# Optimization experiments

Hardware: AMD Instinct MI355X
Metric: run time of the kernel (lower is better)

The kernel has to match this reference:

```python
import jax, jax.numpy as jnp
import numpy as np

B, L, E, DA, R = 256, 2048, 64, 64, 32

def setup_inputs() -> dict:
    key = jax.random.key(0)
    k1, k2, k3, k4 = jax.random.split(key, 4)
    x = jax.random.normal(k1, (B, L, E), dtype=jnp.float32)
    mask = (jax.random.uniform(k2, (B, L)) > 0.2).astype(jnp.float32)
    # glorot-uniform-like init for the small attention weights
    lim1 = np.sqrt(6.0 / (DA + E)).astype(np.float32)
    lim2 = np.sqrt(6.0 / (R + DA)).astype(np.float32)
    W1 = jax.random.uniform(k3, (DA, E), minval=-lim1, maxval=lim1, dtype=jnp.float32)
    W2 = jax.random.uniform(k4, (R, DA), minval=-lim2, maxval=lim2, dtype=jnp.float32)
    return {"x": x, "mask": mask, "W1": W1, "W2": W2}

def reference(x, mask, W1, W2):
    # x: (B,L,E), mask: (B,L), W1: (DA,E), W2: (R,DA)
    xm = x * mask[:, :, None]                       # masked inputs (B,L,E)
    H = jnp.tanh(jnp.einsum('de,ble->bdl', W1, xm))  # (B,DA,L)
    Q = jnp.einsum('rd,bdl->brl', W2, H)             # (B,R,L)
    A = jnp.exp(Q) * mask[:, None, :]                # masked exp scores (B,R,L)
    A = A / jnp.sum(A, axis=2, keepdims=True)        # normalize over L
    # dropout is identity at inference
    return jnp.einsum('brl,ble->bre', A, xm)         # (B,R,E)
```

## Files before the change

kernel.cpp:

```cpp
#include <hip/hip_runtime.h>
#include <hip/hip_bf16.h>


#define B_  256
#define L_  2048
#define E_  64
#define DA_ 64
#define R_  32
#define CH_ 8
#define TL_ 128
#define NS_ 2

typedef __attribute__((ext_vector_type(8))) short bf16x8;
typedef __attribute__((ext_vector_type(4))) float f32x4;

#define XS_WROW 36
#define XT_WROW 68
#define AS_WROW 68
#define XS_WORDS (TL_ * XS_WROW)
#define XT_WORDS (E_ * XT_WROW)
#define AS_WORDS (R_ * AS_WROW)

__device__ __forceinline__ unsigned pk(float a, float b) {
    __hip_bfloat162 h = __float22bfloat162_rn(float2{a, b});
    union { __hip_bfloat162 h2; unsigned u; } cv; cv.h2 = h;
    return cv.u;
}
__device__ __forceinline__ float bflo(unsigned u) { return __uint_as_float(u << 16); }
__device__ __forceinline__ float bfhi(unsigned u) { return __uint_as_float(u & 0xFFFF0000u); }
__device__ __forceinline__ float fast_tanh(float v) {
    float e = __expf(2.0f * v);
    return 1.0f - 2.0f / (e + 1.0f);
}

__launch_bounds__(256, 3)
__global__ void selfbi_main(const float* __restrict__ x,
                            const float* __restrict__ mask,
                            const float* __restrict__ W1,
                            const float* __restrict__ W2,
                            float* __restrict__ accp,
                            float* __restrict__ ssump) {
    __shared__ unsigned smem[XS_WORDS + XT_WORDS + AS_WORDS + TL_];
    unsigned* xsw = smem;
    unsigned* xtw = smem + XS_WORDS;
    unsigned* asw = xtw + XT_WORDS;
    float*    ms  = (float*)(asw + AS_WORDS);

    const int b   = blockIdx.x;
    const int c   = blockIdx.y;
    const int tid = threadIdx.x;
    const int w    = tid >> 6;
    const int lane = tid & 63;
    const int g    = lane >> 4;
    const int ml   = lane & 15;

    bf16x8 w1f[4][2], w2f[2][2];
    #pragma unroll
    for (int mt = 0; mt < 4; ++mt)
        #pragma unroll
        for (int kb = 0; kb < 2; ++kb) {
            const float* p = W1 + (16 * mt + ml) * E_ + 32 * kb + 8 * g;
            float4 a = *(const float4*)p, bb = *(const float4*)(p + 4);
            union { bf16x8 s; unsigned u[4]; } cv;
            cv.u[0] = pk(a.x, a.y); cv.u[1] = pk(a.z, a.w);
            cv.u[2] = pk(bb.x, bb.y); cv.u[3] = pk(bb.z, bb.w);
            w1f[mt][kb] = cv.s;
        }
    #pragma unroll
    for (int mt = 0; mt < 2; ++mt)
        #pragma unroll
        for (int kb = 0; kb < 2; ++kb) {
            const float* p = W2 + (16 * mt + ml) * DA_ + 32 * kb + 8 * g;
            float4 a = *(const float4*)p, bb = *(const float4*)(p + 4);
            union { bf16x8 s; unsigned u[4]; } cv;
            cv.u[0] = pk(a.x, a.y); cv.u[1] = pk(a.z, a.w);
            cv.u[2] = pk(bb.x, bb.y); cv.u[3] = pk(bb.z, bb.w);
            w2f[mt][kb] = cv.s;
        }

    f32x4 c3[2] = {f32x4{0,0,0,0}, f32x4{0,0,0,0}};
    float ssum_acc = 0.0f;

    for (int s = 0; s < NS_; ++s) {
        if (s) __syncthreads();

        {
            const int t = tid >> 1, half = tid & 1;
            const int gl = b * L_ + c * (NS_ * TL_) + s * TL_ + t;
            const float m = mask[gl];
            if (!half) ms[t] = m;
            const float4* xr = (const float4*)(x + (size_t)gl * E_ + half * 32);
            float v[32];
            #pragma unroll
            for (int i = 0; i < 8; ++i) {
                float4 q = xr[i];
                v[4*i] = q.x * m; v[4*i+1] = q.y * m; v[4*i+2] = q.z * m; v[4*i+3] = q.w * m;
            }
            #pragma unroll
            for (int i = 0; i < 4; ++i) {
                uint4 u;
                u.x = pk(v[8*i+0], v[8*i+1]); u.y = pk(v[8*i+2], v[8*i+3]);
                u.z = pk(v[8*i+4], v[8*i+5]); u.w = pk(v[8*i+6], v[8*i+7]);
                *(uint4*)&xsw[t * XS_WROW + half * 16 + 4 * i] = u;
            }
            #pragma unroll
            for (int j = 0; j < 32; ++j) {
                const int e = 32 * half + j;
                const int word = e * XT_WROW + ((t >> 1) ^ (half << 4));
                ((__hip_bfloat16*)&xtw[word])[t & 1] = __float2bfloat16(v[j]);
            }
        }

        f32x4 c1[2][4];
        #pragma unroll
        for (int nt = 0; nt < 2; ++nt)
            #pragma unroll
            for (int mt = 0; mt < 4; ++mt) c1[nt][mt] = f32x4{0,0,0,0};
        #pragma unroll
        for (int kb = 0; kb < 2; ++kb)
            #pragma unroll
            for (int nt = 0; nt < 2; ++nt) {
                const int t = 32 * w + 16 * nt + ml;
                bf16x8 bfrag = *(bf16x8*)&xsw[t * XS_WROW + kb * 16 + 4 * g];
                #pragma unroll
                for (int mt = 0; mt < 4; ++mt)
                    c1[nt][mt] = __builtin_amdgcn_mfma_f32_16x16x32_bf16(
                        w1f[mt][kb], bfrag, c1[nt][mt], 0, 0, 0);
            }

        #pragma unroll
        for (int nt = 0; nt < 2; ++nt) {
            const int t = 32 * w + 16 * nt + ml;
            const int sw = 4 * (t & 7);
            #pragma unroll
            for (int mt = 0; mt < 4; ++mt) {
                float h0 = fast_tanh(c1[nt][mt][0]);
                float h1 = fast_tanh(c1[nt][mt][1]);
                float h2 = fast_tanh(c1[nt][mt][2]);
                float h3 = fast_tanh(c1[nt][mt][3]);
                const int d2 = 8 * mt + 2 * g;
                uint2 u; u.x = pk(h0, h1); u.y = pk(h2, h3);
                *(uint2*)&xsw[t * XS_WROW + (d2 ^ sw)] = u;
            }
        }

        f32x4 c2[2][2];
        #pragma unroll
        for (int nt = 0; nt < 2; ++nt)
            #pragma unroll
            for (int mt = 0; mt < 2; ++mt) c2[nt][mt] = f32x4{0,0,0,0};
        #pragma unroll
        for (int kb = 0; kb < 2; ++kb)
            #pragma unroll
            for (int nt = 0; nt < 2; ++nt) {
                const int t = 32 * w + 16 * nt + ml;
                const int sw = 4 * (t & 7);
                bf16x8 bfrag = *(bf16x8*)&xsw[t * XS_WROW + ((16 * kb + 4 * g) ^ sw)];
                #pragma unroll
                for (int mt = 0; mt < 2; ++mt)
                    c2[nt][mt] = __builtin_amdgcn_mfma_f32_16x16x32_bf16(
                        w2f[mt][kb], bfrag, c2[nt][mt], 0, 0, 0);
            }

        #pragma unroll
        for (int nt = 0; nt < 2; ++nt) {
            const int t = 32 * w + 16 * nt + ml;
            const float mval = ms[t];
            const int tw = (t >> 1) ^ (8 * g);
            #pragma unroll
            for (int mt = 0; mt < 2; ++mt)
                #pragma unroll
                for (int reg = 0; reg < 4; ++reg) {
                    const int r = 16 * mt + 4 * g + reg;
                    float a = __expf(c2[nt][mt][reg]) * mval;
                    ((__hip_bfloat16*)&asw[r * AS_WROW + tw])[t & 1] = __float2bfloat16(a);
                }
        }

        __syncthreads();

        {
            const int fx = (w >> 1) << 4;
            const int e  = 16 * w + ml;
            const int phi = 8 * ((ml >> 2) & 3);
            #pragma unroll
            for (int kb = 0; kb < 4; ++kb) {
                bf16x8 bfrag = *(bf16x8*)&xtw[e * XT_WROW + ((16 * kb + 4 * g) ^ fx)];
                #pragma unroll
                for (int mt = 0; mt < 2; ++mt) {
                    const int r = 16 * mt + ml;
                    bf16x8 afrag = *(bf16x8*)&asw[r * AS_WROW + ((16 * kb + 4 * g) ^ phi)];
                    c3[mt] = __builtin_amdgcn_mfma_f32_16x16x32_bf16(
                        afrag, bfrag, c3[mt], 0, 0, 0);
                }
            }
        }

        {
            const int rr = tid >> 3, to = tid & 7;
            const int p2 = (rr >> 2) & 3;
            const int wb = rr * AS_WROW + 8 * (to ^ p2);
            uint4 u0 = *(uint4*)&asw[wb];
            uint4 u1 = *(uint4*)&asw[wb + 4];
            float sv = bflo(u0.x) + bfhi(u0.x) + bflo(u0.y) + bfhi(u0.y)
                     + bflo(u0.z) + bfhi(u0.z) + bflo(u0.w) + bfhi(u0.w)
                     + bflo(u1.x) + bfhi(u1.x) + bflo(u1.y) + bfhi(u1.y)
                     + bflo(u1.z) + bfhi(u1.z) + bflo(u1.w) + bfhi(u1.w);
            ssum_acc += sv;
        }
    }

    float sv = ssum_acc;
    sv += __shfl_xor(sv, 1); sv += __shfl_xor(sv, 2); sv += __shfl_xor(sv, 4);

    const size_t obase = (size_t)(b * CH_ + c) * (R_ * E_);
    const int e = 16 * w + ml;
    #pragma unroll
    for (int mt = 0; mt < 2; ++mt)
        #pragma unroll
        for (int reg = 0; reg < 4; ++reg) {
            const int r = 16 * mt + 4 * g + reg;
            accp[obase + r * E_ + e] = c3[mt][reg];
        }
    if ((tid & 7) == 0) ssump[(b * CH_ + c) * R_ + (tid >> 3)] = sv;
}

__launch_bounds__(256, 4)
__global__ void selfbi_reduce(const float* __restrict__ accp,
                              const float* __restrict__ ssump,
                              float* __restrict__ out) {
    const int of = blockIdx.x * 256 + threadIdx.x;
    const int b  = of >> 11;
    const int o  = of & 2047;
    const int r  = o >> 6;
    float num = 0.f, den = 0.f;
    #pragma unroll
    for (int cc = 0; cc < CH_; ++cc) {
        num += accp[((size_t)(b * CH_ + cc)) * (R_ * E_) + o];
        den += ssump[(b * CH_ + cc) * R_ + r];
    }
    out[of] = num / den;
}

extern "C" void kernel_launch(void* const* d_in, const int* in_sizes, int n_in,
                              void* d_out, int out_size, void* d_ws, size_t ws_size,
                              hipStream_t stream) {
    const float* x    = (const float*)d_in[0];
    const float* mask = (const float*)d_in[1];
    const float* W1   = (const float*)d_in[2];
    const float* W2   = (const float*)d_in[3];
    float* out        = (float*)d_out;

    float* accp  = (float*)d_ws;
    float* ssump = accp + (size_t)B_ * CH_ * R_ * E_;

    selfbi_main<<<dim3(B_, CH_), dim3(256), 0, stream>>>(x, mask, W1, W2, accp, ssump);
    selfbi_reduce<<<dim3((B_ * R_ * E_) / 256), dim3(256), 0, stream>>>(accp, ssump, out);
}
```

Baseline: 219.8 us.

## Load x fragments directly to registers and restructure score GEMM layout

After: 227.0 us. +3.3%, slower.

```diff
diff --git a/kernel.cpp b/kernel.cpp
--- a/kernel.cpp
+++ b/kernel.cpp
@@ -8,18 +8,18 @@
 #define DA_ 64
 #define R_  32
 #define CH_ 8
-#define TL_ 128
 #define NS_ 2
 
 typedef __attribute__((ext_vector_type(8))) short bf16x8;
 typedef __attribute__((ext_vector_type(4))) float f32x4;
 
-#define XS_WROW 36
-#define XT_WROW 68
-#define AS_WROW 68
-#define XS_WORDS (TL_ * XS_WROW)
-#define XT_WORDS (E_ * XT_WROW)
-#define AS_WORDS (R_ * AS_WROW)
+#define HS_P 36
+#define XT_P 68
+#define AS_P 68
+#define HS_W (128 * HS_P)
+#define XT_W (64 * XT_P)
+#define AS_W (32 * AS_P)
+#define SS_W (32 * 16)
 
 __device__ __forceinline__ unsigned pk(float a, float b) {
     __hip_bfloat162 h = __float22bfloat162_rn(float2{a, b});
@@ -29,8 +29,12 @@
 __device__ __forceinline__ float bflo(unsigned u) { return __uint_as_float(u << 16); }
 __device__ __forceinline__ float bfhi(unsigned u) { return __uint_as_float(u & 0xFFFF0000u); }
 __device__ __forceinline__ float fast_tanh(float v) {
-    float e = __expf(2.0f * v);
-    return 1.0f - 2.0f / (e + 1.0f);
+    float e = __builtin_amdgcn_exp2f(v * 2.885390082f);
+    float r = __builtin_amdgcn_rcpf(e + 1.0f);
+    return fmaf(-2.0f, r, 1.0f);
+}
+__device__ __forceinline__ float fast_exp(float v) {
+    return __builtin_amdgcn_exp2f(v * 1.442695041f);
 }
 
 __launch_bounds__(256, 3)
@@ -40,19 +44,21 @@
                             const float* __restrict__ W2,
                             float* __restrict__ accp,
                             float* __restrict__ ssump) {
-    __shared__ unsigned smem[XS_WORDS + XT_WORDS + AS_WORDS + TL_];
-    unsigned* xsw = smem;
-    unsigned* xtw = smem + XS_WORDS;
-    unsigned* asw = xtw + XT_WORDS;
-    float*    ms  = (float*)(asw + AS_WORDS);
-
-    const int b   = blockIdx.x;
-    const int c   = blockIdx.y;
-    const int tid = threadIdx.x;
+    __shared__ __align__(16) unsigned smem[HS_W + XT_W + AS_W + SS_W];
+    unsigned* hsw = smem;
+    unsigned* xtw = smem + HS_W;
+    unsigned* asw = xtw + XT_W;
+    float*    ssp = (float*)(asw + AS_W);
+
+    const int b    = blockIdx.x;
+    const int c    = blockIdx.y;
+    const int tid  = threadIdx.x;
     const int w    = tid >> 6;
     const int lane = tid & 63;
     const int g    = lane >> 4;
     const int ml   = lane & 15;
+    const int p4   = tid & 31;
+    const int q8   = tid >> 5;
 
     bf16x8 w1f[4][2], w2f[2][2];
     #pragma unroll
@@ -67,15 +73,15 @@
             w1f[mt][kb] = cv.s;
         }
     #pragma unroll
-    for (int mt = 0; mt < 2; ++mt)
+    for (int nt = 0; nt < 2; ++nt)
         #pragma unroll
         for (int kb = 0; kb < 2; ++kb) {
-            const float* p = W2 + (16 * mt + ml) * DA_ + 32 * kb + 8 * g;
+            const float* p = W2 + (16 * nt + ml) * DA_ + 32 * kb + 8 * g;
             float4 a = *(const float4*)p, bb = *(const float4*)(p + 4);
             union { bf16x8 s; unsigned u[4]; } cv;
             cv.u[0] = pk(a.x, a.y); cv.u[1] = pk(a.z, a.w);
             cv.u[2] = pk(bb.x, bb.y); cv.u[3] = pk(bb.z, bb.w);
-            w2f[mt][kb] = cv.s;
+            w2f[nt][kb] = cv.s;
         }
 
     f32x4 c3[2] = {f32x4{0,0,0,0}, f32x4{0,0,0,0}};
@@ -84,33 +90,51 @@
     for (int s = 0; s < NS_; ++s) {
         if (s) __syncthreads();
 
-        {
-            const int t = tid >> 1, half = tid & 1;
-            const int gl = b * L_ + c * (NS_ * TL_) + s * TL_ + t;
-            const float m = mask[gl];
-            if (!half) ms[t] = m;
-            const float4* xr = (const float4*)(x + (size_t)gl * E_ + half * 32);
-            float v[32];
-            #pragma unroll
-            for (int i = 0; i < 8; ++i) {
-                float4 q = xr[i];
-                v[4*i] = q.x * m; v[4*i+1] = q.y * m; v[4*i+2] = q.z * m; v[4*i+3] = q.w * m;
-            }
-            #pragma unroll
-            for (int i = 0; i < 4; ++i) {
-                uint4 u;
-                u.x = pk(v[8*i+0], v[8*i+1]); u.y = pk(v[8*i+2], v[8*i+3]);
-                u.z = pk(v[8*i+4], v[8*i+5]); u.w = pk(v[8*i+6], v[8*i+7]);
-                *(uint4*)&xsw[t * XS_WROW + half * 16 + 4 * i] = u;
-            }
-            #pragma unroll
-            for (int j = 0; j < 32; ++j) {
-                const int e = 32 * half + j;
-                const int word = e * XT_WROW + ((t >> 1) ^ (half << 4));
-                ((__hip_bfloat16*)&xtw[word])[t & 1] = __float2bfloat16(v[j]);
-            }
-        }
-
+        const int    l0    = c * (NS_ * 128) + s * 128;
+        const size_t xbase = ((size_t)b * L_ + l0) * E_;
+
+        float xe[4][8];
+        #pragma unroll
+        for (int k = 0; k < 4; ++k) {
+            const float* p = x + xbase + (size_t)(4 * p4 + k) * E_ + 8 * q8;
+            float4 a = *(const float4*)p, bb = *(const float4*)(p + 4);
+            xe[k][0] = a.x;  xe[k][1] = a.y;  xe[k][2] = a.z;  xe[k][3] = a.w;
+            xe[k][4] = bb.x; xe[k][5] = bb.y; xe[k][6] = bb.z; xe[k][7] = bb.w;
+        }
+        float4 gb[2][2][2];
+        #pragma unroll
+        for (int nt = 0; nt < 2; ++nt)
+            #pragma unroll
+            for (int kb = 0; kb < 2; ++kb) {
+                const float* p = x + xbase + (size_t)(32 * w + 16 * nt + ml) * E_
+                                 + 32 * kb + 8 * g;
+                gb[nt][kb][0] = *(const float4*)p;
+                gb[nt][kb][1] = *(const float4*)(p + 4);
+            }
+        float4 mk[2];
+        #pragma unroll
+        for (int mt = 0; mt < 2; ++mt)
+            mk[mt] = *(const float4*)(mask + b * L_ + l0 + 32 * w + 16 * mt + 4 * g);
+
+        #pragma unroll
+        for (int j = 0; j < 8; ++j) {
+            uint2 u;
+            u.x = pk(xe[0][j], xe[1][j]);
+            u.y = pk(xe[2][j], xe[3][j]);
+            *(uint2*)&xtw[(8 * q8 + j) * XT_P + 2 * p4] = u;
+        }
+
+        bf16x8 xf[2][2];
+        #pragma unroll
+        for (int nt = 0; nt < 2; ++nt)
+            #pragma unroll
+            for (int kb = 0; kb < 2; ++kb) {
+                union { bf16x8 s; unsigned u[4]; } cv;
+                float4 a = gb[nt][kb][0], bb = gb[nt][kb][1];
+                cv.u[0] = pk(a.x, a.y); cv.u[1] = pk(a.z, a.w);
+                cv.u[2] = pk(bb.x, bb.y); cv.u[3] = pk(bb.z, bb.w);
+                xf[nt][kb] = cv.s;
+            }
         f32x4 c1[2][4];
         #pragma unroll
         for (int nt = 0; nt < 2; ++nt)
@@ -119,99 +143,82 @@
         #pragma unroll
         for (int kb = 0; kb < 2; ++kb)
             #pragma unroll
-            for (int nt = 0; nt < 2; ++nt) {
-                const int t = 32 * w + 16 * nt + ml;
-                bf16x8 bfrag = *(bf16x8*)&xsw[t * XS_WROW + kb * 16 + 4 * g];
+            for (int nt = 0; nt < 2; ++nt)
                 #pragma unroll
                 for (int mt = 0; mt < 4; ++mt)
                     c1[nt][mt] = __builtin_amdgcn_mfma_f32_16x16x32_bf16(
-                        w1f[mt][kb], bfrag, c1[nt][mt], 0, 0, 0);
-            }
+                        w1f[mt][kb], xf[nt][kb], c1[nt][mt], 0, 0, 0);
 
         #pragma unroll
         for (int nt = 0; nt < 2; ++nt) {
             const int t = 32 * w + 16 * nt + ml;
-            const int sw = 4 * (t & 7);
             #pragma unroll
             for (int mt = 0; mt < 4; ++mt) {
                 float h0 = fast_tanh(c1[nt][mt][0]);
                 float h1 = fast_tanh(c1[nt][mt][1]);
                 float h2 = fast_tanh(c1[nt][mt][2]);
                 float h3 = fast_tanh(c1[nt][mt][3]);
-                const int d2 = 8 * mt + 2 * g;
                 uint2 u; u.x = pk(h0, h1); u.y = pk(h2, h3);
-                *(uint2*)&xsw[t * XS_WROW + (d2 ^ sw)] = u;
+                *(uint2*)&hsw[t * HS_P + 8 * mt + 2 * g] = u;
             }
         }
 
         f32x4 c2[2][2];
         #pragma unroll
-        for (int nt = 0; nt < 2; ++nt)
-            #pragma unroll
-            for (int mt = 0; mt < 2; ++mt) c2[nt][mt] = f32x4{0,0,0,0};
+        for (int mt = 0; mt < 2; ++mt)
+            #pragma unroll
+            for (int nt = 0; nt < 2; ++nt) c2[mt][nt] = f32x4{0,0,0,0};
         #pragma unroll
         for (int kb = 0; kb < 2; ++kb)
             #pragma unroll
+            for (int mt = 0; mt < 2; ++mt) {
+                bf16x8 af = *(bf16x8*)&hsw[(32 * w + 16 * mt + ml) * HS_P
+                                           + 16 * kb + 4 * g];
+                #pragma unroll
+                for (int nt = 0; nt < 2; ++nt)
+                    c2[mt][nt] = __builtin_amdgcn_mfma_f32_16x16x32_bf16(
+                        af, w2f[nt][kb], c2[mt][nt], 0, 0, 0);
+            }
+
+        float part[2] = {0.f, 0.f};
+        #pragma unroll
+        for (int mt = 0; mt < 2; ++mt) {
+            const float m0 = mk[mt].x, m1 = mk[mt].y, m2 = mk[mt].z, m3 = mk[mt].w;
+            const int tw = 16 * w + 8 * mt + 2 * g;
+            #pragma unroll
             for (int nt = 0; nt < 2; ++nt) {
-                const int t = 32 * w + 16 * nt + ml;
-                const int sw = 4 * (t & 7);
-                bf16x8 bfrag = *(bf16x8*)&xsw[t * XS_WROW + ((16 * kb + 4 * g) ^ sw)];
-                #pragma unroll
-                for (int mt = 0; mt < 2; ++mt)
-                    c2[nt][mt] = __builtin_amdgcn_mfma_f32_16x16x32_bf16(
-                        w2f[mt][kb], bfrag, c2[nt][mt], 0, 0, 0);
-            }
-
-        #pragma unroll
-        for (int nt = 0; nt < 2; ++nt) {
-            const int t = 32 * w + 16 * nt + ml;
-            const float mval = ms[t];
-            const int tw = (t >> 1) ^ (8 * g);
-            #pragma unroll
-            for (int mt = 0; mt < 2; ++mt)
-                #pragma unroll
-                for (int reg = 0; reg < 4; ++reg) {
-                    const int r = 16 * mt + 4 * g + reg;
-                    float a = __expf(c2[nt][mt][reg]) * mval;
-                    ((__hip_bfloat16*)&asw[r * AS_WROW + tw])[t & 1] = __float2bfloat16(a);
-                }
-        }
+                float a0 = fast_exp(c2[mt][nt][0]) * m0;
+                float a1 = fast_exp(c2[mt][nt][1]) * m1;
+                float a2 = fast_exp(c2[mt][nt][2]) * m2;
+                float a3 = fast_exp(c2[mt][nt][3]) * m3;
+                uint2 u; u.x = pk(a0, a1); u.y = pk(a2, a3);
+                *(uint2*)&asw[(16 * nt + ml) * AS_P + tw] = u;
+                part[nt] += bflo(u.x) + bfhi(u.x) + bflo(u.y) + bfhi(u.y);
+            }
+        }
+        #pragma unroll
+        for (int nt = 0; nt < 2; ++nt)
+            ssp[(16 * nt + ml) * 16 + 4 * w + g] = part[nt];
 
         __syncthreads();
 
-        {
-            const int fx = (w >> 1) << 4;
-            const int e  = 16 * w + ml;
-            const int phi = 8 * ((ml >> 2) & 3);
-            #pragma unroll
-            for (int kb = 0; kb < 4; ++kb) {
-                bf16x8 bfrag = *(bf16x8*)&xtw[e * XT_WROW + ((16 * kb + 4 * g) ^ fx)];
-                #pragma unroll
-                for (int mt = 0; mt < 2; ++mt) {
-                    const int r = 16 * mt + ml;
-                    bf16x8 afrag = *(bf16x8*)&asw[r * AS_WROW + ((16 * kb + 4 * g) ^ phi)];
-                    c3[mt] = __builtin_amdgcn_mfma_f32_16x16x32_bf16(
-                        afrag, bfrag, c3[mt], 0, 0, 0);
-                }
-            }
-        }
-
-        {
-            const int rr = tid >> 3, to = tid & 7;
-            const int p2 = (rr >> 2) & 3;
-            const int wb = rr * AS_WROW + 8 * (to ^ p2);
-            uint4 u0 = *(uint4*)&asw[wb];
-            uint4 u1 = *(uint4*)&asw[wb + 4];
-            float sv = bflo(u0.x) + bfhi(u0.x) + bflo(u0.y) + bfhi(u0.y)
-                     + bflo(u0.z) + bfhi(u0.z) + bflo(u0.w) + bfhi(u0.w)
-                     + bflo(u1.x) + bfhi(u1.x) + bflo(u1.y) + bfhi(u1.y)
-                     + bflo(u1.z) + bfhi(u1.z) + bflo(u1.w) + bfhi(u1.w);
-            ssum_acc += sv;
+        #pragma unroll
+        for (int kb = 0; kb < 4; ++kb) {
+            bf16x8 bf = *(bf16x8*)&xtw[(16 * w + ml) * XT_P + 16 * kb + 4 * g];
+            #pragma unroll
+            for (int mt = 0; mt < 2; ++mt) {
+                bf16x8 af = *(bf16x8*)&asw[(16 * mt + ml) * AS_P + 16 * kb + 4 * g];
+                c3[mt] = __builtin_amdgcn_mfma_f32_16x16x32_bf16(af, bf, c3[mt], 0, 0, 0);
+            }
+        }
+
+        if (tid < 32) {
+            const float4* q = (const float4*)&ssp[tid * 16];
+            float4 q0 = q[0], q1 = q[1], q2 = q[2], q3 = q[3];
+            ssum_acc += (q0.x + q0.y + q0.z + q0.w) + (q1.x + q1.y + q1.z + q1.w)
+                      + (q2.x + q2.y + q2.z + q2.w) + (q3.x + q3.y + q3.z + q3.w);
         }
     }
-
-    float sv = ssum_acc;
-    sv += __shfl_xor(sv, 1); sv += __shfl_xor(sv, 2); sv += __shfl_xor(sv, 4);
 
     const size_t obase = (size_t)(b * CH_ + c) * (R_ * E_);
     const int e = 16 * w + ml;
@@ -222,7 +229,7 @@
             const int r = 16 * mt + 4 * g + reg;
             accp[obase + r * E_ + e] = c3[mt][reg];
         }
-    if ((tid & 7) == 0) ssump[(b * CH_ + c) * R_ + (tid >> 3)] = sv;
+    if (tid < 32) ssump[(b * CH_ + c) * R_ + tid] = ssum_acc;
 }
 
 __launch_bounds__(256, 4)
```
